# Optimization experiments

Measured on AMD Instinct MI355X. Metric: run time of the kernel, lower is better.

Reference implementation:

```python
import jax, jax.numpy as jnp
import numpy as np

B, S, D, H = 2, 2048, 2048, 16
DH = D // H
NEG = -1000000000.0


def setup_inputs() -> dict:
    key = jax.random.key(0)
    ks = jax.random.split(key, 5)
    return {
        "query_vector": jax.random.normal(ks[0], (B, S, D), dtype=jnp.float32),
        "key_vector": jax.random.normal(ks[1], (B, S, D), dtype=jnp.float32),
        "value_vector": jax.random.normal(ks[2], (B, S, D), dtype=jnp.float32),
        "W_qkv": jax.random.normal(ks[3], (D, 3 * D), dtype=jnp.float32) * (1.0 / np.sqrt(D)),
        "b_qkv": jax.random.normal(ks[4], (3 * D,), dtype=jnp.float32) * 0.01,
    }


def reference(query_vector, key_vector, value_vector, W_qkv, b_qkv):
    # NOTE: original forward only consumes query_vector; key/value args unused.
    qkv = query_vector @ W_qkv + b_qkv                      # [B, S, 3D]
    q, k, v = jnp.split(qkv, 3, axis=-1)                    # each [B, S, D]
    # Faithful to original: plain reshape (NOT transpose) into heads.
    q = q.reshape(B, H, S, DH)
    k = k.reshape(B, H, S, DH)
    v = v.reshape(B, H, S, DH)
    scores = jnp.einsum("bhqd,bhkd->bhqk", q, k) / np.float32(np.sqrt(DH))
    # torch.triu_indices(offset=0): mask j >= i (diagonal included), SET to -1e9.
    idx = jnp.arange(S)
    causal = idx[None, :] >= idx[:, None]                   # [S, S], True where masked
    scores = jnp.where(causal, jnp.float32(NEG), scores)
    attn = jax.nn.softmax(scores, axis=-1)
    out = jnp.einsum("bhqk,bhkd->bhqd", attn, v)            # [B, H, S, DH]
    # dropout is identity in eval mode
    return out.reshape(B, S, D)
```

## Files before the change

kernel.cpp:

```cpp
#include <hip/hip_runtime.h>
#include <hip/hip_bf16.h>
#include <stdint.h>

typedef unsigned short u16;
typedef short short8 __attribute__((ext_vector_type(8)));
typedef short short4v __attribute__((ext_vector_type(4)));
typedef float f32x4 __attribute__((ext_vector_type(4)));

#define CSL (0.08838834764831845f * 1.4426950408889634f)
#define NEGR -1.0e13f


__device__ __forceinline__ u16 f2b(float f) {
  union { float f; unsigned int u; } c; c.f = f;
  unsigned int u = c.u;
  u += 0x7fffu + ((u >> 16) & 1u);
  return (u16)(u >> 16);
}
__device__ __forceinline__ float b2f(u16 h) {
  union { float f; unsigned int u; } c; c.u = ((unsigned int)h) << 16;
  return c.f;
}

__global__ __launch_bounds__(256) void k_cast_fused(const float* __restrict__ q_in,
                                                    u16* __restrict__ qbf,
                                                    const float* __restrict__ W,
                                                    u16* __restrict__ Wt) {
  __shared__ u16 L[64 * 68];
  const int t = threadIdx.x;
  const int b = blockIdx.x;
  if (b < 4096) {
    size_t idx = ((size_t)b * 256 + t) * 8;
    float4 f0 = *(const float4*)(q_in + idx);
    float4 f1 = *(const float4*)(q_in + idx + 4);
    short8 o;
    o[0] = (short)f2b(f0.x); o[1] = (short)f2b(f0.y); o[2] = (short)f2b(f0.z); o[3] = (short)f2b(f0.w);
    o[4] = (short)f2b(f1.x); o[5] = (short)f2b(f1.y); o[6] = (short)f2b(f1.z); o[7] = (short)f2b(f1.w);
    *(short8*)(qbf + idx) = o;
    return;
  }
  const int wb = b - 4096;
  const int nb = (wb % 96) * 64;
  const int kb = (wb / 96) * 64;
#pragma unroll
  for (int it = 0; it < 4; ++it) {
    int idx = it * 1024 + t * 4;
    int r = idx >> 6, c = idx & 63;
    float4 f = *(const float4*)(W + (size_t)(kb + r) * 6144 + nb + c);
    L[r * 68 + c + 0] = f2b(f.x);
    L[r * 68 + c + 1] = f2b(f.y);
    L[r * 68 + c + 2] = f2b(f.z);
    L[r * 68 + c + 3] = f2b(f.w);
  }
  __syncthreads();
#pragma unroll
  for (int it = 0; it < 4; ++it) {
    int idx = it * 1024 + t * 4;
    int i = idx >> 6, j = idx & 63;
    short4v o;
#pragma unroll
    for (int e = 0; e < 4; ++e) o[e] = (short)L[(j + e) * 68 + i];
    *(short4v*)(Wt + (size_t)(nb + i) * 2048 + kb + j) = o;
  }
}

__global__ __launch_bounds__(512, 4) void k_gemm128(const u16* __restrict__ A,
                                                    const u16* __restrict__ Bt,
                                                    const float* __restrict__ bias,
                                                    u16* __restrict__ qb,
                                                    u16* __restrict__ kbuf,
                                                    u16* __restrict__ vbuf) {
  __shared__ u16 As[2][8192];
  __shared__ u16 Bs[2][12288];
  const int t = threadIdx.x;
  const int ln = t & 63, w = t >> 6;
  const int lr = ln & 15, lg = ln >> 4;
  const int wm = w >> 2, wn = w & 3;
  const int Lid = blockIdx.x;
  const int xcd = Lid & 7, l = Lid >> 3;
  const int mt = (xcd & 1) * 16 + (l & 15);
  const int nt = (xcd >> 1) * 8 + (l >> 4);
  const int mb = mt * 128, nb = nt * 192;
  const int cswz = (lr & 7) * 8;
  const int srow = w * 8 + (ln >> 3);
  const int scol = ((ln & 7) ^ (ln >> 3)) * 8;

  const u16* Abase = A + (size_t)mb * 2048;
  const u16* Bbase = Bt + (size_t)nb * 2048;

  f32x4 acc[4][3] = {};

#define STAGE_KT(kt_, buf_)                                                                        \
  do {                                                                                             \
    const u16* as_ = Abase + (size_t)srow * 2048 + (kt_) * 64 + scol;                              \
    const u16* bs_ = Bbase + (size_t)srow * 2048 + (kt_) * 64 + scol;                              \
    _Pragma("unroll")                                                                              \
    for (int p = 0; p < 2; ++p)                                                                    \
      __builtin_amdgcn_global_load_lds(                                                            \
          (const __attribute__((address_space(1))) void*)(as_ + (size_t)p * 64 * 2048),            \
          (__attribute__((address_space(3))) void*)(&As[buf_][p * 4096 + w * 512]), 16, 0, 0);     \
    _Pragma("unroll")                                                                              \
    for (int p = 0; p < 3; ++p)                                                                    \
      __builtin_amdgcn_global_load_lds(                                                            \
          (const __attribute__((address_space(1))) void*)(bs_ + (size_t)p * 64 * 2048),            \
          (__attribute__((address_space(3))) void*)(&Bs[buf_][p * 4096 + w * 512]), 16, 0, 0);     \
  } while (0)

  STAGE_KT(0, 0);
  asm volatile("s_waitcnt vmcnt(0)" ::: "memory");
  __builtin_amdgcn_s_barrier();

  for (int kt = 0; kt < 32; ++kt) {
    const int cur = kt & 1;
    const int ktn = (kt + 1) & 31;
    const u16* At = &As[cur][0];
    const u16* Bl = &Bs[cur][0];

    STAGE_KT(ktn, cur ^ 1);
    asm volatile("s_waitcnt vmcnt(5)" ::: "memory");
    __builtin_amdgcn_s_barrier();

    short8 af[4][2], bf[3][2];
#pragma unroll
    for (int mi = 0; mi < 4; ++mi)
#pragma unroll
      for (int ks = 0; ks < 2; ++ks)
        af[mi][ks] = *(const short8*)(At + (wm * 64 + mi * 16 + lr) * 64 + ((ks * 32 + lg * 8) ^ cswz));
#pragma unroll
    for (int ni = 0; ni < 3; ++ni)
#pragma unroll
      for (int ks = 0; ks < 2; ++ks)
        bf[ni][ks] = *(const short8*)(Bl + (wn * 48 + ni * 16 + lr) * 64 + ((ks * 32 + lg * 8) ^ cswz));

    __builtin_amdgcn_s_setprio(1);
#pragma unroll
    for (int ks = 0; ks < 2; ++ks)
#pragma unroll
      for (int mi = 0; mi < 4; ++mi)
#pragma unroll
        for (int ni = 0; ni < 3; ++ni)
          acc[mi][ni] = __builtin_amdgcn_mfma_f32_16x16x32_bf16(af[mi][ks], bf[ni][ks], acc[mi][ni], 0, 0, 0);
    __builtin_amdgcn_s_setprio(0);
    __builtin_amdgcn_s_barrier();
  }
#undef STAGE_KT
  asm volatile("s_waitcnt vmcnt(0)" ::: "memory");

#pragma unroll
  for (int ni = 0; ni < 3; ++ni) {
    int ncol = nb + wn * 48 + ni * 16 + lr;
    u16* dst = (ncol < 2048) ? qb : (ncol < 4096 ? kbuf : vbuf);
    int nmod = ncol & 2047;
    float bv = bias[ncol];
#pragma unroll
    for (int mi = 0; mi < 4; ++mi) {
#pragma unroll
      for (int r = 0; r < 4; ++r) {
        int mrow = mb + wm * 64 + mi * 16 + lg * 4 + r;
        dst[(size_t)mrow * 2048 + nmod] = f2b(acc[mi][ni][r] + bv);
      }
    }
  }
}

__global__ __launch_bounds__(256) void k_vtrans(const u16* __restrict__ v, u16* __restrict__ vt,
                                                float* __restrict__ part) {
  __shared__ u16 L[128 * 136];
  __shared__ float Ls2[256];
  const int t = threadIdx.x;
  const int bh = blockIdx.y, sc = blockIdx.x;
  const size_t base = (size_t)bh * 262144;
#pragma unroll
  for (int it = 0; it < 8; ++it) {
    int chunk = it * 256 + t;
    int s = chunk >> 4, d8 = (chunk & 15) * 8;
    *(short8*)(L + s * 136 + d8) = *(const short8*)(v + base + (size_t)(sc * 128 + s) * 128 + d8);
  }
  __syncthreads();
#pragma unroll
  for (int it = 0; it < 8; ++it) {
    int chunk = it * 256 + t;
    int dh = chunk >> 4, s8 = (chunk & 15) * 8;
    short8 o;
#pragma unroll
    for (int e = 0; e < 8; ++e) o[e] = (short)L[(s8 + e) * 136 + dh];
    *(short8*)(vt + base + (size_t)dh * 2048 + sc * 128 + s8) = o;
  }
  {
    const int dh = t & 127, seg = t >> 7;
    float ps = 0.f;
#pragma unroll 8
    for (int i = 0; i < 64; ++i) ps += b2f(L[(seg * 64 + i) * 136 + dh]);
    Ls2[t] = ps;
    __syncthreads();
    if (t < 128) part[((size_t)bh * 16 + sc) * 128 + t] = Ls2[t] + Ls2[t + 128];
  }
}

__global__ __launch_bounds__(256, 3) void k_attn(const u16* __restrict__ qb,
                                                 const u16* __restrict__ kb,
                                                 const u16* __restrict__ vt,
                                                 const float* __restrict__ part,
                                                 float* __restrict__ out) {
  __shared__ u16 Ks[64 * 128];
  __shared__ u16 Vs[128 * 64];
  __shared__ u16 Ps[4][16 * 64];
  const int t = threadIdx.x;
  const int ln = t & 63, wv = t >> 6;
  const int lr = ln & 15, lg = ln >> 4;
  const int lr7 = lr & 7;
  const int L = blockIdx.y * 32 + blockIdx.x;
  const int wl = (L & 7) * 128 + (L >> 3);
  const int bh = wl >> 5;
  const int qt = 31 - (wl & 31);
  const size_t base = (size_t)bh * 262144;
  const u16* Qh = qb + base;
  const u16* Kh = kb + base;
  const u16* Vth = vt + base;
  float* Oh = out + base;
  const int qs = qt * 64;

  short8 qf[4];
  {
    int qr = qs + wv * 16 + lr;
#pragma unroll
    for (int ks = 0; ks < 4; ++ks)
      qf[ks] = *(const short8*)(Qh + (size_t)qr * 128 + ks * 32 + lg * 8);
  }
  float lsum[4] = {0.f, 0.f, 0.f, 0.f};
  f32x4 acc[8];
  const f32x4 fz = {0.f, 0.f, 0.f, 0.f};
#pragma unroll
  for (int oj = 0; oj < 8; ++oj) acc[oj] = fz;

  u16* Pw = &Ps[wv][0];
  const int nkt = qt + 1;
  for (int kt = 0; kt < nkt; ++kt) {
#pragma unroll
    for (int it = 0; it < 4; ++it) {
      int chunk = it * 256 + wv * 64 + ln;
      int sk = chunk >> 4, c8 = (chunk & 15) ^ (sk & 7);
      __builtin_amdgcn_global_load_lds(
          (const __attribute__((address_space(1))) void*)(Kh + (size_t)(kt * 64 + sk) * 128 + c8 * 8),
          (__attribute__((address_space(3))) void*)(Ks + (size_t)(it * 256 + wv * 64) * 8),
          16, 0, 0);
    }
#pragma unroll
    for (int it = 0; it < 4; ++it) {
      int chunk = it * 256 + wv * 64 + ln;
      int dh = chunk >> 3, c8 = (chunk & 7) ^ (dh & 7);
      __builtin_amdgcn_global_load_lds(
          (const __attribute__((address_space(1))) void*)(Vth + (size_t)dh * 2048 + kt * 64 + c8 * 8),
          (__attribute__((address_space(3))) void*)(Vs + (size_t)(it * 256 + wv * 64) * 8),
          16, 0, 0);
    }
    __syncthreads();

    f32x4 s[4];
#pragma unroll
    for (int ni = 0; ni < 4; ++ni) s[ni] = fz;
#pragma unroll
    for (int ks = 0; ks < 4; ++ks) {
#pragma unroll
      for (int ni = 0; ni < 4; ++ni) {
        short8 kf = *(const short8*)(Ks + (ni * 16 + lr) * 128 + ((ks * 4 + lg) ^ lr7) * 8);
        s[ni] = __builtin_amdgcn_mfma_f32_16x16x32_bf16(qf[ks], kf, s[ni], 0, 0, 0);
      }
    }
    if (kt == qt) {
#pragma unroll
      for (int ni = 0; ni < 4; ++ni) {
        int col = kt * 64 + ni * 16 + lr;
#pragma unroll
        for (int r = 0; r < 4; ++r) {
          int row = qs + wv * 16 + lg * 4 + r;
          if (col >= row) s[ni][r] = NEGR;
        }
      }
    }
#pragma unroll
    for (int ni = 0; ni < 4; ++ni)
#pragma unroll
      for (int r = 0; r < 4; ++r) {
        u16 h = f2b(exp2f(s[ni][r] * CSL));
        int pr = lg * 4 + r, pc = ni * 16 + lr;
        Pw[pr * 64 + ((pc >> 3) ^ (pr & 7)) * 8 + (pc & 7)] = h;
        lsum[r] += b2f(h);
      }
#pragma unroll
    for (int ks2 = 0; ks2 < 2; ++ks2) {
      short8 pa = *(const short8*)(Pw + lr * 64 + ((ks2 * 4 + lg) ^ lr7) * 8);
#pragma unroll
      for (int oj = 0; oj < 8; ++oj) {
        short8 vf = *(const short8*)(Vs + (oj * 16 + lr) * 64 + ((ks2 * 4 + lg) ^ lr7) * 8);
        acc[oj] = __builtin_amdgcn_mfma_f32_16x16x32_bf16(pa, vf, acc[oj], 0, 0, 0);
      }
    }
    __syncthreads();
  }

  float rl[4];
#pragma unroll
  for (int r = 0; r < 4; ++r) {
    float sa = lsum[r];
#pragma unroll
    for (int d = 1; d < 16; d <<= 1) sa += __shfl_xor(sa, d, 64);
    rl[r] = 1.0f / sa;
  }
#pragma unroll
  for (int oj = 0; oj < 8; ++oj)
#pragma unroll
    for (int r = 0; r < 4; ++r) {
      int row = qs + wv * 16 + lg * 4 + r;
      float val = acc[oj][r] * rl[r];
      if (qt == 0 && wv == 0 && lg == 0 && r == 0) {
        float vs = 0.f;
#pragma unroll
        for (int sc = 0; sc < 16; ++sc) vs += part[(size_t)bh * 2048 + sc * 128 + oj * 16 + lr];
        val = vs * (1.0f / 2048.0f);
      }
      Oh[(size_t)row * 128 + oj * 16 + lr] = val;
    }
}

extern "C" void kernel_launch(void* const* d_in, const int* in_sizes, int n_in,
                              void* d_out, int out_size, void* d_ws, size_t ws_size,
                              hipStream_t stream) {
  (void)in_sizes; (void)n_in; (void)out_size; (void)ws_size;
  const float* q_in = (const float*)d_in[0];
  const float* W = (const float*)d_in[3];
  const float* bias = (const float*)d_in[4];
  float* out = (float*)d_out;

  u16* qbf = (u16*)d_ws;
  u16* wtb = qbf + (size_t)4096 * 2048;
  u16* qb  = wtb + (size_t)6144 * 2048;
  u16* kbf = qb  + (size_t)4096 * 2048;
  u16* vbf = kbf + (size_t)4096 * 2048;
  u16* vt  = vbf + (size_t)4096 * 2048;
  float* part = (float*)(vt + (size_t)4096 * 2048);

  k_cast_fused<<<7168, 256, 0, stream>>>(q_in, qbf, W, wtb);
  k_gemm128<<<1024, 512, 0, stream>>>(qbf, wtb, bias, qb, kbf, vbf);
  k_vtrans<<<dim3(16, 32), 256, 0, stream>>>(vbf, vt, part);
  k_attn<<<dim3(32, 32), 256, 0, stream>>>(qb, kbf, vt, part, out);
}
```

Measured before the change: 218.8 us.

## Fuse V transpose into QKV GEMM epilogue and drop separate transpose kernel

The GEMM epilogue now writes the V third of the projection straight into the head-transposed [bh][d][s] layout. This removes the intermediate V buffer and the shared-memory transpose kernel. A lighter kernel reads the transposed V and computes the per-chunk column sums the attention kernel needs. The trade-off is that the V epilogue stores become 2-byte writes with large strides between lanes, which coalesce poorly and may offset the saved memory traffic.

```diff
diff --git a/kernel.cpp b/kernel.cpp
--- a/kernel.cpp
+++ b/kernel.cpp
@@ -69,7 +69,7 @@
                                                     const float* __restrict__ bias,
                                                     u16* __restrict__ qb,
                                                     u16* __restrict__ kbuf,
-                                                    u16* __restrict__ vbuf) {
+                                                    u16* __restrict__ vt) {
   __shared__ u16 As[2][8192];
   __shared__ u16 Bs[2][12288];
   const int t = threadIdx.x;
@@ -149,52 +149,51 @@
 #pragma unroll
   for (int ni = 0; ni < 3; ++ni) {
     int ncol = nb + wn * 48 + ni * 16 + lr;
-    u16* dst = (ncol < 2048) ? qb : (ncol < 4096 ? kbuf : vbuf);
-    int nmod = ncol & 2047;
     float bv = bias[ncol];
-#pragma unroll
-    for (int mi = 0; mi < 4; ++mi) {
-#pragma unroll
-      for (int r = 0; r < 4; ++r) {
-        int mrow = mb + wm * 64 + mi * 16 + lg * 4 + r;
-        dst[(size_t)mrow * 2048 + nmod] = f2b(acc[mi][ni][r] + bv);
-      }
-    }
-  }
-}
-
-__global__ __launch_bounds__(256) void k_vtrans(const u16* __restrict__ v, u16* __restrict__ vt,
-                                                float* __restrict__ part) {
-  __shared__ u16 L[128 * 136];
-  __shared__ float Ls2[256];
+    if (ncol < 4096) {
+      u16* dst = (ncol < 2048) ? qb : kbuf;
+      int nmod = ncol & 2047;
+#pragma unroll
+      for (int mi = 0; mi < 4; ++mi) {
+#pragma unroll
+        for (int r = 0; r < 4; ++r) {
+          int mrow = mb + wm * 64 + mi * 16 + lg * 4 + r;
+          dst[(size_t)mrow * 2048 + nmod] = f2b(acc[mi][ni][r] + bv);
+        }
+      }
+    } else {
+      int nmod = ncol - 4096;
+      int d = nmod & 127, shi = nmod >> 7;
+#pragma unroll
+      for (int mi = 0; mi < 4; ++mi) {
+#pragma unroll
+        for (int r = 0; r < 4; ++r) {
+          int mrow = mb + wm * 64 + mi * 16 + lg * 4 + r;
+          int bh = mrow >> 7;
+          int rl = mrow & 127;
+          vt[((size_t)bh << 18) + (size_t)d * 2048 + rl * 16 + shi] = f2b(acc[mi][ni][r] + bv);
+        }
+      }
+    }
+  }
+}
+
+__global__ __launch_bounds__(256) void k_vpart(const u16* __restrict__ vt, float* __restrict__ part) {
+  __shared__ float L[256];
   const int t = threadIdx.x;
-  const int bh = blockIdx.y, sc = blockIdx.x;
-  const size_t base = (size_t)bh * 262144;
-#pragma unroll
-  for (int it = 0; it < 8; ++it) {
-    int chunk = it * 256 + t;
-    int s = chunk >> 4, d8 = (chunk & 15) * 8;
-    *(short8*)(L + s * 136 + d8) = *(const short8*)(v + base + (size_t)(sc * 128 + s) * 128 + d8);
-  }
+  const int sc = blockIdx.x, bh = blockIdx.y;
+  const int d = t >> 1, half = t & 1;
+  const u16* p = vt + ((size_t)bh << 18) + (size_t)d * 2048 + sc * 128 + half * 64;
+  float s = 0.f;
+#pragma unroll
+  for (int i = 0; i < 8; ++i) {
+    short8 v = *(const short8*)(p + i * 8);
+#pragma unroll
+    for (int e = 0; e < 8; ++e) s += b2f((u16)v[e]);
+  }
+  L[t] = s;
   __syncthreads();
-#pragma unroll
-  for (int it = 0; it < 8; ++it) {
-    int chunk = it * 256 + t;
-    int dh = chunk >> 4, s8 = (chunk & 15) * 8;
-    short8 o;
-#pragma unroll
-    for (int e = 0; e < 8; ++e) o[e] = (short)L[(s8 + e) * 136 + dh];
-    *(short8*)(vt + base + (size_t)dh * 2048 + sc * 128 + s8) = o;
-  }
-  {
-    const int dh = t & 127, seg = t >> 7;
-    float ps = 0.f;
-#pragma unroll 8
-    for (int i = 0; i < 64; ++i) ps += b2f(L[(seg * 64 + i) * 136 + dh]);
-    Ls2[t] = ps;
-    __syncthreads();
-    if (t < 128) part[((size_t)bh * 16 + sc) * 128 + t] = Ls2[t] + Ls2[t + 128];
-  }
+  if (half == 0) part[((size_t)bh * 16 + sc) * 128 + d] = L[t] + L[t + 1];
 }
 
 __global__ __launch_bounds__(256, 3) void k_attn(const u16* __restrict__ qb,
@@ -336,12 +335,11 @@
   u16* wtb = qbf + (size_t)4096 * 2048;
   u16* qb  = wtb + (size_t)6144 * 2048;
   u16* kbf = qb  + (size_t)4096 * 2048;
-  u16* vbf = kbf + (size_t)4096 * 2048;
-  u16* vt  = vbf + (size_t)4096 * 2048;
+  u16* vt  = kbf + (size_t)4096 * 2048;
   float* part = (float*)(vt + (size_t)4096 * 2048);
 
   k_cast_fused<<<7168, 256, 0, stream>>>(q_in, qbf, W, wtb);
-  k_gemm128<<<1024, 512, 0, stream>>>(qbf, wtb, bias, qb, kbf, vbf);
-  k_vtrans<<<dim3(16, 32), 256, 0, stream>>>(vbf, vt, part);
+  k_gemm128<<<1024, 512, 0, stream>>>(qbf, wtb, bias, qb, kbf, vt);
+  k_vpart<<<dim3(16, 32), 256, 0, stream>>>(vt, part);
   k_attn<<<dim3(32, 32), 256, 0, stream>>>(qb, kbf, vt, part, out);
 }
```

New measurement: 362.8 us. 65.8% more time.
